# Kernel tuning notes

Hardware: AMD Instinct MI355X
Metric: run time of the kernel (lower is better)

The kernel has to match this reference:

```python
import jax, jax.numpy as jnp
import numpy as np

B, N, K, H, NI = 8, 4096, 32, 128, 384
SCALE = 30.0
EPS = 1e-5


def _ln(x, g, b):
    m = jnp.mean(x, axis=-1, keepdims=True)
    v = jnp.mean(jnp.square(x - m), axis=-1, keepdims=True)
    return (x - m) * jax.lax.rsqrt(v + EPS) * g + b


def setup_inputs() -> dict:
    key = jax.random.key(0)
    ks = jax.random.split(key, 20)
    w = lambda k, shape: jax.random.normal(k, shape, jnp.float32) * 0.02
    return {
        "h_V": jax.random.normal(ks[0], (B, N, H), jnp.float32),
        "h_E": jax.random.normal(ks[1], (B, N, K, NI), jnp.float32),
        "mask_V": (jax.random.uniform(ks[2], (B, N)) > 0.1).astype(jnp.float32),
        "mask_attend": (jax.random.uniform(ks[3], (B, N, K)) > 0.1).astype(jnp.float32),
        "W1_w": w(ks[4], (H, H + NI)), "W1_b": jnp.zeros((H,), jnp.float32),
        "W2_w": w(ks[5], (H, H)), "W2_b": jnp.zeros((H,), jnp.float32),
        "W3_w": w(ks[6], (H, H)), "W3_b": jnp.zeros((H,), jnp.float32),
        "ln1_g": jnp.ones((H,), jnp.float32), "ln1_b": jnp.zeros((H,), jnp.float32),
        "ln2_g": jnp.ones((H,), jnp.float32), "ln2_b": jnp.zeros((H,), jnp.float32),
        "Win_w": w(ks[7], (4 * H, H)), "Win_b": jnp.zeros((4 * H,), jnp.float32),
        "Wout_w": w(ks[8], (H, 4 * H)), "Wout_b": jnp.zeros((H,), jnp.float32),
    }


def reference(h_V, h_E, mask_V, mask_attend,
              W1_w, W1_b, W2_w, W2_b, W3_w, W3_b,
              ln1_g, ln1_b, ln2_g, ln2_b,
              Win_w, Win_b, Wout_w, Wout_b):
    gelu = lambda x: jax.nn.gelu(x, approximate=False)  # torch exact GELU
    # Split W1 across the broadcast (h_V) and per-edge (h_E) inputs instead of
    # materializing the [B,N,K,H+NI] concat: identical math, less memory.
    W1v, W1e = W1_w[:, :H], W1_w[:, H:]
    hv_part = jnp.einsum('bnh,oh->bno', h_V, W1v)              # [B,N,H]
    he_part = jnp.einsum('bnke,oe->bnko', h_E, W1e)            # [B,N,K,H]
    m = gelu(hv_part[:, :, None, :] + he_part + W1_b)
    m = gelu(jnp.einsum('bnkh,oh->bnko', m, W2_w) + W2_b)
    m = jnp.einsum('bnkh,oh->bnko', m, W3_w) + W3_b            # h_message
    m = mask_attend[..., None] * m
    dh = jnp.sum(m, axis=-2) / SCALE                           # [B,N,H]
    h = _ln(h_V + dh, ln1_g, ln1_b)
    ff = jnp.einsum('bnf,of->bno', gelu(jnp.einsum('bnh,fh->bnf', h, Win_w) + Win_b), Wout_w) + Wout_b
    h = _ln(h + ff, ln2_g, ln2_b)
    return mask_V[..., None] * h
```

## Files before the change

### kernel.cpp

```cpp
#include <hip/hip_runtime.h>

#define NODES 32768

typedef __attribute__((ext_vector_type(8))) short bf16x8;
typedef __attribute__((ext_vector_type(4))) float f32x4;

__device__ __forceinline__ unsigned short f2bf(float f) {
  __bf16 b = (__bf16)f;
  return __builtin_bit_cast(unsigned short, b);
}

__device__ __forceinline__ float gelu_f(float x) {
  float e = __builtin_amdgcn_exp2f(-2.4558673f * x);
  return x * __builtin_amdgcn_rcpf(1.0f + e);
}

__device__ __forceinline__ f32x4 mfma16(bf16x8 a, bf16x8 b, f32x4 c) {
  return __builtin_amdgcn_mfma_f32_16x16x32_bf16(a, b, c, 0, 0, 0);
}

__global__ void DecLayer_54357106098674_kernel() {}

__global__ __launch_bounds__(256) void pack_kernel(
    const float* __restrict__ W, unsigned short* __restrict__ out,
    int ctiles, int ld) {
  int ct = blockIdx.x % ctiles;
  int ks = blockIdx.x / ctiles;
#pragma unroll
  for (int h = 0; h < 2; ++h) {
    int idx = threadIdx.x + h * 256;
    int j = idx & 7;
    int lane = idx >> 3;
    int o = ct * 16 + (lane & 15);
    int k = ks * 32 + ((lane >> 4) << 3) + j;
    out[((size_t)blockIdx.x * 64 + lane) * 8 + j] = f2bf(W[(size_t)o * ld + k]);
  }
}

__global__ __launch_bounds__(256, 3) void edge_kernel(
    const float* __restrict__ hE, const float* __restrict__ hV,
    const float* __restrict__ maskA,
    const unsigned short* __restrict__ W1p,
    const unsigned short* __restrict__ W2p,
    const unsigned short* __restrict__ W3p,
    const float* __restrict__ W1bias,
    const float* __restrict__ W2bias, const float* __restrict__ W3bias,
    const float* __restrict__ ln1g, const float* __restrict__ ln1b,
    float* __restrict__ hb) {
  __shared__ __align__(16) unsigned short A[64 * 392];
  __shared__ __align__(16) unsigned short hvb[2][136];
  __shared__ float mkl[64];
  unsigned short* m1 = A;
  unsigned short* m2 = A + 8704;
  float* red2 = (float*)(A + 17408);

  const int t = threadIdx.x;
  const int pair = ((blockIdx.x & 7) << 11) | (blockIdx.x >> 3);
  const int node0 = pair * 2;
  const float* vb0 = hV + (size_t)node0 * 128;
  const float* vb1 = vb0 + 128;

  {
    const int rr = t >> 3, cc = t & 7;
    const f32x4* src = (const f32x4*)(hE + (size_t)node0 * 12288) + rr * 96 + cc;
    unsigned short* dst0 = &A[rr * 392 + cc * 4];
#pragma unroll
    for (int i = 0; i < 12; ++i) {
      f32x4 v = __builtin_nontemporal_load(src + i * 8);
      ushort4 u;
      u.x = f2bf(v[0]); u.y = f2bf(v[1]); u.z = f2bf(v[2]); u.w = f2bf(v[3]);
      *(ushort4*)(dst0 + i * 32) = u;
    }
    const f32x4* src1 = src + 32 * 96;
    unsigned short* dst1 = &A[(rr + 32) * 392 + cc * 4];
#pragma unroll
    for (int i = 0; i < 12; ++i) {
      f32x4 v = __builtin_nontemporal_load(src1 + i * 8);
      ushort4 u;
      u.x = f2bf(v[0]); u.y = f2bf(v[1]); u.z = f2bf(v[2]); u.w = f2bf(v[3]);
      *(ushort4*)(dst1 + i * 32) = u;
    }
  }
  if (t < 64) {
    int nn = t >> 5, s = t & 31;
    f32x4 v = ((const f32x4*)(hV + (size_t)(node0 + nn) * 128))[s];
    ushort4 u;
    u.x = f2bf(v[0]); u.y = f2bf(v[1]); u.z = f2bf(v[2]); u.w = f2bf(v[3]);
    *(ushort4*)&hvb[nn][s * 4] = u;
  } else if (t < 128) {
    int q = t - 64;
    mkl[q] = maskA[(size_t)node0 * 32 + q];
  }
  __syncthreads();

  const int w = t >> 6, l = t & 63, lr = l & 15, lk = l >> 4;
  const int ct0 = w * 2, ct1 = w * 2 + 1;
  const int c0 = ct0 * 16 + lr, c1 = ct1 * 16 + lr;

  f32x4 g0[4], g1[4];
#pragma unroll
  for (int rt = 0; rt < 4; ++rt) {
    g0[rt] = (f32x4){0.f, 0.f, 0.f, 0.f};
    g1[rt] = (f32x4){0.f, 0.f, 0.f, 0.f};
  }
#pragma unroll
  for (int ks = 0; ks < 16; ++ks) {
    bf16x8 w0 = *(const bf16x8*)&W1p[((size_t)(ks * 8 + ct0) * 64 + l) * 8];
    bf16x8 w1 = *(const bf16x8*)&W1p[((size_t)(ks * 8 + ct1) * 64 + l) * 8];
#pragma unroll
    for (int rt = 0; rt < 4; ++rt) {
      bf16x8 a;
      if (ks < 4)
        a = *(const bf16x8*)&hvb[rt >> 1][ks * 32 + lk * 8];
      else
        a = *(const bf16x8*)&A[(rt * 16 + lr) * 392 + (ks - 4) * 32 + lk * 8];
      g0[rt] = mfma16(a, w0, g0[rt]);
      g1[rt] = mfma16(a, w1, g1[rt]);
    }
  }
  __syncthreads();

  {
    float bb0 = W1bias[c0], bb1 = W1bias[c1];
#pragma unroll
    for (int rt = 0; rt < 4; ++rt) {
#pragma unroll
      for (int r = 0; r < 4; ++r) {
        int row = rt * 16 + lk * 4 + r;
        m1[row * 136 + c0] = f2bf(gelu_f(g0[rt][r] + bb0));
        m1[row * 136 + c1] = f2bf(gelu_f(g1[rt][r] + bb1));
      }
    }
  }
  __syncthreads();

  f32x4 d0[4], d1[4];
#pragma unroll
  for (int rt = 0; rt < 4; ++rt) {
    d0[rt] = (f32x4){0.f, 0.f, 0.f, 0.f};
    d1[rt] = (f32x4){0.f, 0.f, 0.f, 0.f};
  }
#pragma unroll
  for (int ks = 0; ks < 4; ++ks) {
    bf16x8 w0 = *(const bf16x8*)&W2p[((size_t)(ks * 8 + ct0) * 64 + l) * 8];
    bf16x8 w1 = *(const bf16x8*)&W2p[((size_t)(ks * 8 + ct1) * 64 + l) * 8];
#pragma unroll
    for (int rt = 0; rt < 4; ++rt) {
      bf16x8 a = *(const bf16x8*)&m1[(rt * 16 + lr) * 136 + ks * 32 + lk * 8];
      d0[rt] = mfma16(a, w0, d0[rt]);
      d1[rt] = mfma16(a, w1, d1[rt]);
    }
  }
  {
    float bb0 = W2bias[c0], bb1 = W2bias[c1];
#pragma unroll
    for (int rt = 0; rt < 4; ++rt) {
#pragma unroll
      for (int r = 0; r < 4; ++r) {
        int row = rt * 16 + lk * 4 + r;
        m2[row * 136 + c0] = f2bf(gelu_f(d0[rt][r] + bb0));
        m2[row * 136 + c1] = f2bf(gelu_f(d1[rt][r] + bb1));
      }
    }
  }
  __syncthreads();

  f32x4 e0[4], e1[4];
#pragma unroll
  for (int rt = 0; rt < 4; ++rt) {
    e0[rt] = (f32x4){0.f, 0.f, 0.f, 0.f};
    e1[rt] = (f32x4){0.f, 0.f, 0.f, 0.f};
  }
#pragma unroll
  for (int ks = 0; ks < 4; ++ks) {
    bf16x8 w0 = *(const bf16x8*)&W3p[((size_t)(ks * 8 + ct0) * 64 + l) * 8];
    bf16x8 w1 = *(const bf16x8*)&W3p[((size_t)(ks * 8 + ct1) * 64 + l) * 8];
#pragma unroll
    for (int rt = 0; rt < 4; ++rt) {
      bf16x8 a = *(const bf16x8*)&m2[(rt * 16 + lr) * 136 + ks * 32 + lk * 8];
      e0[rt] = mfma16(a, w0, e0[rt]);
      e1[rt] = mfma16(a, w1, e1[rt]);
    }
  }

  {
    float b30 = W3bias[c0], b31 = W3bias[c1];
    float cs00 = 0.f, cs01 = 0.f, cs10 = 0.f, cs11 = 0.f;
#pragma unroll
    for (int r = 0; r < 4; ++r) {
      float mka = mkl[lk * 4 + r];
      float mkb = mkl[16 + lk * 4 + r];
      float mkc = mkl[32 + lk * 4 + r];
      float mkd = mkl[48 + lk * 4 + r];
      cs00 += mka * (e0[0][r] + b30) + mkb * (e0[1][r] + b30);
      cs01 += mka * (e1[0][r] + b31) + mkb * (e1[1][r] + b31);
      cs10 += mkc * (e0[2][r] + b30) + mkd * (e0[3][r] + b30);
      cs11 += mkc * (e1[2][r] + b31) + mkd * (e1[3][r] + b31);
    }
    cs00 += __shfl_xor(cs00, 16); cs00 += __shfl_xor(cs00, 32);
    cs01 += __shfl_xor(cs01, 16); cs01 += __shfl_xor(cs01, 32);
    cs10 += __shfl_xor(cs10, 16); cs10 += __shfl_xor(cs10, 32);
    cs11 += __shfl_xor(cs11, 16); cs11 += __shfl_xor(cs11, 32);
    if (lk == 0) {
      red2[c0]       = vb0[c0] + cs00 * (1.0f / 30.0f);
      red2[c1]       = vb0[c1] + cs01 * (1.0f / 30.0f);
      red2[128 + c0] = vb1[c0] + cs10 * (1.0f / 30.0f);
      red2[128 + c1] = vb1[c1] + cs11 * (1.0f / 30.0f);
    }
  }
  __syncthreads();

  {
    const int nn = w >> 1, ww = w & 1;
    const float* rn = red2 + nn * 128;
    float v0 = rn[l], v1 = rn[l + 64];
    float s = v0 + v1, sq = v0 * v0 + v1 * v1;
#pragma unroll
    for (int off = 1; off < 64; off <<= 1) {
      s += __shfl_xor(s, off);
      sq += __shfl_xor(sq, off);
    }
    float mean = s * (1.0f / 128.0f);
    float var = sq * (1.0f / 128.0f) - mean * mean;
    float rs = rsqrtf(var + 1e-5f);
    size_t ob = (size_t)(node0 + nn) * 128;
    if (ww == 0)
      hb[ob + l] = (v0 - mean) * rs * ln1g[l] + ln1b[l];
    else
      hb[ob + 64 + l] = (v1 - mean) * rs * ln1g[64 + l] + ln1b[64 + l];
  }
}

__global__ __launch_bounds__(256) void ffn_kernel(
    const float* h,
    const unsigned short* __restrict__ Winp,
    const unsigned short* __restrict__ Woutp,
    const float* __restrict__ Winbias, const float* __restrict__ Woutbias,
    const float* __restrict__ ln2g, const float* __restrict__ ln2b,
    const float* __restrict__ maskV, float* out) {
  __shared__ __align__(16) unsigned short hA[32 * 136];
  __shared__ __align__(16) unsigned short tl[32 * 520];
  __shared__ float mn[32], rstd[32], mv[32];
  float* ol = (float*)tl;

  const int t = threadIdx.x;
  const size_t base = (size_t)blockIdx.x * 32 * 128;

#pragma unroll
  for (int i = 0; i < 4; ++i) {
    int q = t + i * 256;
    int row = q >> 5, c4 = q & 31;
    f32x4 v = ((const f32x4*)(h + base))[q];
    ushort4 u;
    u.x = f2bf(v[0]); u.y = f2bf(v[1]); u.z = f2bf(v[2]); u.w = f2bf(v[3]);
    *(ushort4*)&hA[row * 136 + c4 * 4] = u;
  }
  if (t < 32) mv[t] = maskV[(size_t)blockIdx.x * 32 + t];
  __syncthreads();

  const int w = t >> 6, l = t & 63, lr = l & 15, lk = l >> 4;

  f32x4 p0[8], p1[8];
#pragma unroll
  for (int j = 0; j < 8; ++j) { p0[j] = (f32x4){0.f,0.f,0.f,0.f}; p1[j] = (f32x4){0.f,0.f,0.f,0.f}; }
#pragma unroll
  for (int ks = 0; ks < 4; ++ks) {
    bf16x8 a0 = *(const bf16x8*)&hA[lr * 136 + ks * 32 + lk * 8];
    bf16x8 a1 = *(const bf16x8*)&hA[(16 + lr) * 136 + ks * 32 + lk * 8];
#pragma unroll
    for (int j = 0; j < 8; ++j) {
      bf16x8 bv = *(const bf16x8*)&Winp[((size_t)(ks * 32 + (w * 8 + j)) * 64 + l) * 8];
      p0[j] = mfma16(a0, bv, p0[j]);
      p1[j] = mfma16(a1, bv, p1[j]);
    }
  }
#pragma unroll
  for (int j = 0; j < 8; ++j) {
    int col = (w * 8 + j) * 16 + lr;
    float bb = Winbias[col];
#pragma unroll
    for (int r = 0; r < 4; ++r) {
      tl[(lk * 4 + r) * 520 + col] = f2bf(gelu_f(p0[j][r] + bb));
      tl[(16 + lk * 4 + r) * 520 + col] = f2bf(gelu_f(p1[j][r] + bb));
    }
  }
  __syncthreads();

  const int ct0 = w * 2, ct1 = w * 2 + 1;
  const int c0 = ct0 * 16 + lr, c1 = ct1 * 16 + lr;
  f32x4 d00 = {0.f,0.f,0.f,0.f}, d01 = {0.f,0.f,0.f,0.f};
  f32x4 d10 = {0.f,0.f,0.f,0.f}, d11 = {0.f,0.f,0.f,0.f};
#pragma unroll
  for (int ks = 0; ks < 16; ++ks) {
    bf16x8 a0 = *(const bf16x8*)&tl[lr * 520 + ks * 32 + lk * 8];
    bf16x8 a1 = *(const bf16x8*)&tl[(16 + lr) * 520 + ks * 32 + lk * 8];
    bf16x8 w0 = *(const bf16x8*)&Woutp[((size_t)(ks * 8 + ct0) * 64 + l) * 8];
    bf16x8 w1 = *(const bf16x8*)&Woutp[((size_t)(ks * 8 + ct1) * 64 + l) * 8];
    d00 = mfma16(a0, w0, d00);
    d01 = mfma16(a0, w1, d01);
    d10 = mfma16(a1, w0, d10);
    d11 = mfma16(a1, w1, d11);
  }
  __syncthreads();
  {
    float bo0 = Woutbias[c0], bo1 = Woutbias[c1];
#pragma unroll
    for (int r = 0; r < 4; ++r) {
      int r0 = lk * 4 + r, r1 = 16 + lk * 4 + r;
      ol[r0 * 132 + c0] = d00[r] + bo0 + h[base + (size_t)r0 * 128 + c0];
      ol[r0 * 132 + c1] = d01[r] + bo1 + h[base + (size_t)r0 * 128 + c1];
      ol[r1 * 132 + c0] = d10[r] + bo0 + h[base + (size_t)r1 * 128 + c0];
      ol[r1 * 132 + c1] = d11[r] + bo1 + h[base + (size_t)r1 * 128 + c1];
    }
  }
  __syncthreads();

  {
    int row = t >> 3, p = t & 7;
    float s = 0.f, sq = 0.f;
#pragma unroll
    for (int i = 0; i < 16; ++i) {
      float x = ol[row * 132 + p * 16 + i];
      s += x; sq += x * x;
    }
    s += __shfl_xor(s, 1); sq += __shfl_xor(sq, 1);
    s += __shfl_xor(s, 2); sq += __shfl_xor(sq, 2);
    s += __shfl_xor(s, 4); sq += __shfl_xor(sq, 4);
    if (p == 0) {
      float mean = s * (1.0f / 128.0f);
      mn[row] = mean;
      rstd[row] = rsqrtf(sq * (1.0f / 128.0f) - mean * mean + 1e-5f);
    }
  }
  __syncthreads();

#pragma unroll
  for (int i = 0; i < 4; ++i) {
    int q = t + i * 256;
    int row = q >> 5, c = (q & 31) * 4;
    float m_ = mn[row], rs_ = rstd[row], mvv = mv[row];
    const float* orow = &ol[row * 132];
    f32x4 o;
    o[0] = mvv * ((orow[c + 0] - m_) * rs_ * ln2g[c + 0] + ln2b[c + 0]);
    o[1] = mvv * ((orow[c + 1] - m_) * rs_ * ln2g[c + 1] + ln2b[c + 1]);
    o[2] = mvv * ((orow[c + 2] - m_) * rs_ * ln2g[c + 2] + ln2b[c + 2]);
    o[3] = mvv * ((orow[c + 3] - m_) * rs_ * ln2g[c + 3] + ln2b[c + 3]);
    ((f32x4*)(out + base))[q] = o;
  }
}

extern "C" void kernel_launch(void* const* d_in, const int* in_sizes, int n_in,
                              void* d_out, int out_size, void* d_ws, size_t ws_size,
                              hipStream_t stream) {
  (void)in_sizes; (void)n_in; (void)out_size; (void)ws_size;
  const float* h_V   = (const float*)d_in[0];
  const float* h_E   = (const float*)d_in[1];
  const float* maskV = (const float*)d_in[2];
  const float* maskA = (const float*)d_in[3];
  const float* W1w   = (const float*)d_in[4];
  const float* W1b   = (const float*)d_in[5];
  const float* W2w   = (const float*)d_in[6];
  const float* W2b   = (const float*)d_in[7];
  const float* W3w   = (const float*)d_in[8];
  const float* W3b   = (const float*)d_in[9];
  const float* g1    = (const float*)d_in[10];
  const float* b1    = (const float*)d_in[11];
  const float* g2    = (const float*)d_in[12];
  const float* b2    = (const float*)d_in[13];
  const float* Winw  = (const float*)d_in[14];
  const float* Winb  = (const float*)d_in[15];
  const float* Woutw = (const float*)d_in[16];
  const float* Woutb = (const float*)d_in[17];
  float* out = (float*)d_out;

  char* ws = (char*)d_ws;
  unsigned short* W1p   = (unsigned short*)(ws + 0);
  unsigned short* W2p   = (unsigned short*)(ws + 131072);
  unsigned short* W3p   = (unsigned short*)(ws + 163840);
  unsigned short* Winp  = (unsigned short*)(ws + 196608);
  unsigned short* Woutp = (unsigned short*)(ws + 327680);

  pack_kernel<<<128, 256, 0, stream>>>(W1w,   W1p,    8, 512);
  pack_kernel<<<32,  256, 0, stream>>>(W2w,   W2p,    8, 128);
  pack_kernel<<<32,  256, 0, stream>>>(W3w,   W3p,    8, 128);
  pack_kernel<<<128, 256, 0, stream>>>(Winw,  Winp,  32, 128);
  pack_kernel<<<128, 256, 0, stream>>>(Woutw, Woutp,  8, 512);

  edge_kernel<<<NODES / 2, 256, 0, stream>>>(h_E, h_V, maskA, W1p, W2p, W3p,
                                             W1b, W2b, W3b, g1, b1, out);
  ffn_kernel<<<NODES / 32, 256, 0, stream>>>(out, Winp, Woutp, Winb, Woutb,
                                             g2, b2, maskV, out);
}
```

Before: 436.6 us.

## Switch edge MLP h_E, W1e, W2, W3 and activations to FP8 MFMA

```diff
diff --git a/kernel.cpp b/kernel.cpp
--- a/kernel.cpp
+++ b/kernel.cpp
@@ -10,6 +10,16 @@
   return __builtin_bit_cast(unsigned short, b);
 }
 
+__device__ __forceinline__ unsigned char f2fp8(float x) {
+  int v = __builtin_amdgcn_cvt_pk_fp8_f32(x, x, 0, false);
+  return (unsigned char)(v & 0xff);
+}
+__device__ __forceinline__ unsigned int pk4(f32x4 v) {
+  int r = __builtin_amdgcn_cvt_pk_fp8_f32(v[0], v[1], 0, false);
+  r = __builtin_amdgcn_cvt_pk_fp8_f32(v[2], v[3], r, true);
+  return (unsigned int)r;
+}
+
 __device__ __forceinline__ float gelu_f(float x) {
   float e = __builtin_amdgcn_exp2f(-2.4558673f * x);
   return x * __builtin_amdgcn_rcpf(1.0f + e);
@@ -18,12 +28,15 @@
 __device__ __forceinline__ f32x4 mfma16(bf16x8 a, bf16x8 b, f32x4 c) {
   return __builtin_amdgcn_mfma_f32_16x16x32_bf16(a, b, c, 0, 0, 0);
 }
+__device__ __forceinline__ f32x4 mfma8(long a, long b, f32x4 c) {
+  return __builtin_amdgcn_mfma_f32_16x16x32_fp8_fp8(a, b, c, 0, 0, 0);
+}
 
 __global__ void DecLayer_54357106098674_kernel() {}
 
 __global__ __launch_bounds__(256) void pack_kernel(
     const float* __restrict__ W, unsigned short* __restrict__ out,
-    int ctiles, int ld) {
+    int ctiles, int ld, int koff) {
   int ct = blockIdx.x % ctiles;
   int ks = blockIdx.x / ctiles;
 #pragma unroll
@@ -33,26 +46,43 @@
     int lane = idx >> 3;
     int o = ct * 16 + (lane & 15);
     int k = ks * 32 + ((lane >> 4) << 3) + j;
-    out[((size_t)blockIdx.x * 64 + lane) * 8 + j] = f2bf(W[(size_t)o * ld + k]);
-  }
-}
-
-__global__ __launch_bounds__(256, 3) void edge_kernel(
+    out[((size_t)blockIdx.x * 64 + lane) * 8 + j] = f2bf(W[(size_t)o * ld + koff + k]);
+  }
+}
+
+__global__ __launch_bounds__(256) void pack8_kernel(
+    const float* __restrict__ W, unsigned char* __restrict__ out,
+    int ctiles, int ld, int koff) {
+  int ct = blockIdx.x % ctiles;
+  int ks = blockIdx.x / ctiles;
+#pragma unroll
+  for (int h = 0; h < 2; ++h) {
+    int idx = threadIdx.x + h * 256;
+    int j = idx & 7;
+    int lane = idx >> 3;
+    int o = ct * 16 + (lane & 15);
+    int k = ks * 32 + ((lane >> 4) << 3) + j;
+    out[((size_t)blockIdx.x * 64 + lane) * 8 + j] = f2fp8(W[(size_t)o * ld + koff + k]);
+  }
+}
+
+__global__ __launch_bounds__(256, 6) void edge_kernel(
     const float* __restrict__ hE, const float* __restrict__ hV,
     const float* __restrict__ maskA,
-    const unsigned short* __restrict__ W1p,
-    const unsigned short* __restrict__ W2p,
-    const unsigned short* __restrict__ W3p,
+    const unsigned short* __restrict__ W1vp,
+    const unsigned char* __restrict__ W1e8,
+    const unsigned char* __restrict__ W2p8,
+    const unsigned char* __restrict__ W3p8,
     const float* __restrict__ W1bias,
     const float* __restrict__ W2bias, const float* __restrict__ W3bias,
     const float* __restrict__ ln1g, const float* __restrict__ ln1b,
     float* __restrict__ hb) {
-  __shared__ __align__(16) unsigned short A[64 * 392];
+  __shared__ __align__(16) unsigned char A8[64 * 392];
   __shared__ __align__(16) unsigned short hvb[2][136];
   __shared__ float mkl[64];
-  unsigned short* m1 = A;
-  unsigned short* m2 = A + 8704;
-  float* red2 = (float*)(A + 17408);
+  unsigned char* m1 = A8;
+  unsigned char* m2 = A8 + 8704;
+  float* red2 = (float*)(A8 + 17408);
 
   const int t = threadIdx.x;
   const int pair = ((blockIdx.x & 7) << 11) | (blockIdx.x >> 3);
@@ -63,22 +93,18 @@
   {
     const int rr = t >> 3, cc = t & 7;
     const f32x4* src = (const f32x4*)(hE + (size_t)node0 * 12288) + rr * 96 + cc;
-    unsigned short* dst0 = &A[rr * 392 + cc * 4];
+    unsigned char* dst0 = &A8[rr * 392 + cc * 4];
 #pragma unroll
     for (int i = 0; i < 12; ++i) {
       f32x4 v = __builtin_nontemporal_load(src + i * 8);
-      ushort4 u;
-      u.x = f2bf(v[0]); u.y = f2bf(v[1]); u.z = f2bf(v[2]); u.w = f2bf(v[3]);
-      *(ushort4*)(dst0 + i * 32) = u;
+      *(unsigned int*)(dst0 + i * 32) = pk4(v);
     }
     const f32x4* src1 = src + 32 * 96;
-    unsigned short* dst1 = &A[(rr + 32) * 392 + cc * 4];
+    unsigned char* dst1 = &A8[(rr + 32) * 392 + cc * 4];
 #pragma unroll
     for (int i = 0; i < 12; ++i) {
       f32x4 v = __builtin_nontemporal_load(src1 + i * 8);
-      ushort4 u;
-      u.x = f2bf(v[0]); u.y = f2bf(v[1]); u.z = f2bf(v[2]); u.w = f2bf(v[3]);
-      *(ushort4*)(dst1 + i * 32) = u;
+      *(unsigned int*)(dst1 + i * 32) = pk4(v);
     }
   }
   if (t < 64) {
@@ -104,20 +130,27 @@
     g1[rt] = (f32x4){0.f, 0.f, 0.f, 0.f};
   }
 #pragma unroll
-  for (int ks = 0; ks < 16; ++ks) {
-    bf16x8 w0 = *(const bf16x8*)&W1p[((size_t)(ks * 8 + ct0) * 64 + l) * 8];
-    bf16x8 w1 = *(const bf16x8*)&W1p[((size_t)(ks * 8 + ct1) * 64 + l) * 8];
-#pragma unroll
-    for (int rt = 0; rt < 4; ++rt) {
-      bf16x8 a;
-      if (ks < 4)
-        a = *(const bf16x8*)&hvb[rt >> 1][ks * 32 + lk * 8];
-      else
-        a = *(const bf16x8*)&A[(rt * 16 + lr) * 392 + (ks - 4) * 32 + lk * 8];
+  for (int ks = 0; ks < 4; ++ks) {
+    bf16x8 w0 = *(const bf16x8*)&W1vp[((size_t)(ks * 8 + ct0) * 64 + l) * 8];
+    bf16x8 w1 = *(const bf16x8*)&W1vp[((size_t)(ks * 8 + ct1) * 64 + l) * 8];
+#pragma unroll
+    for (int rt = 0; rt < 4; ++rt) {
+      bf16x8 a = *(const bf16x8*)&hvb[rt >> 1][ks * 32 + lk * 8];
       g0[rt] = mfma16(a, w0, g0[rt]);
       g1[rt] = mfma16(a, w1, g1[rt]);
     }
   }
+#pragma unroll
+  for (int ks = 0; ks < 12; ++ks) {
+    long w0 = *(const long*)&W1e8[((size_t)(ks * 8 + ct0) * 64 + l) * 8];
+    long w1 = *(const long*)&W1e8[((size_t)(ks * 8 + ct1) * 64 + l) * 8];
+#pragma unroll
+    for (int rt = 0; rt < 4; ++rt) {
+      long a = *(const long*)&A8[(rt * 16 + lr) * 392 + ks * 32 + lk * 8];
+      g0[rt] = mfma8(a, w0, g0[rt]);
+      g1[rt] = mfma8(a, w1, g1[rt]);
+    }
+  }
   __syncthreads();
 
   {
@@ -127,8 +160,8 @@
 #pragma unroll
       for (int r = 0; r < 4; ++r) {
         int row = rt * 16 + lk * 4 + r;
-        m1[row * 136 + c0] = f2bf(gelu_f(g0[rt][r] + bb0));
-        m1[row * 136 + c1] = f2bf(gelu_f(g1[rt][r] + bb1));
+        m1[row * 136 + c0] = f2fp8(gelu_f(g0[rt][r] + bb0));
+        m1[row * 136 + c1] = f2fp8(gelu_f(g1[rt][r] + bb1));
       }
     }
   }
@@ -142,13 +175,13 @@
   }
 #pragma unroll
   for (int ks = 0; ks < 4; ++ks) {
-    bf16x8 w0 = *(const bf16x8*)&W2p[((size_t)(ks * 8 + ct0) * 64 + l) * 8];
-    bf16x8 w1 = *(const bf16x8*)&W2p[((size_t)(ks * 8 + ct1) * 64 + l) * 8];
-#pragma unroll
-    for (int rt = 0; rt < 4; ++rt) {
-      bf16x8 a = *(const bf16x8*)&m1[(rt * 16 + lr) * 136 + ks * 32 + lk * 8];
-      d0[rt] = mfma16(a, w0, d0[rt]);
-      d1[rt] = mfma16(a, w1, d1[rt]);
+    long w0 = *(const long*)&W2p8[((size_t)(ks * 8 + ct0) * 64 + l) * 8];
+    long w1 = *(const long*)&W2p8[((size_t)(ks * 8 + ct1) * 64 + l) * 8];
+#pragma unroll
+    for (int rt = 0; rt < 4; ++rt) {
+      long a = *(const long*)&m1[(rt * 16 + lr) * 136 + ks * 32 + lk * 8];
+      d0[rt] = mfma8(a, w0, d0[rt]);
+      d1[rt] = mfma8(a, w1, d1[rt]);
     }
   }
   {
@@ -158,8 +191,8 @@
 #pragma unroll
       for (int r = 0; r < 4; ++r) {
         int row = rt * 16 + lk * 4 + r;
-        m2[row * 136 + c0] = f2bf(gelu_f(d0[rt][r] + bb0));
-        m2[row * 136 + c1] = f2bf(gelu_f(d1[rt][r] + bb1));
+        m2[row * 136 + c0] = f2fp8(gelu_f(d0[rt][r] + bb0));
+        m2[row * 136 + c1] = f2fp8(gelu_f(d1[rt][r] + bb1));
       }
     }
   }
@@ -173,13 +206,13 @@
   }
 #pragma unroll
   for (int ks = 0; ks < 4; ++ks) {
-    bf16x8 w0 = *(const bf16x8*)&W3p[((size_t)(ks * 8 + ct0) * 64 + l) * 8];
-    bf16x8 w1 = *(const bf16x8*)&W3p[((size_t)(ks * 8 + ct1) * 64 + l) * 8];
-#pragma unroll
-    for (int rt = 0; rt < 4; ++rt) {
-      bf16x8 a = *(const bf16x8*)&m2[(rt * 16 + lr) * 136 + ks * 32 + lk * 8];
-      e0[rt] = mfma16(a, w0, e0[rt]);
-      e1[rt] = mfma16(a, w1, e1[rt]);
+    long w0 = *(const long*)&W3p8[((size_t)(ks * 8 + ct0) * 64 + l) * 8];
+    long w1 = *(const long*)&W3p8[((size_t)(ks * 8 + ct1) * 64 + l) * 8];
+#pragma unroll
+    for (int rt = 0; rt < 4; ++rt) {
+      long a = *(const long*)&m2[(rt * 16 + lr) * 136 + ks * 32 + lk * 8];
+      e0[rt] = mfma8(a, w0, e0[rt]);
+      e1[rt] = mfma8(a, w1, e1[rt]);
     }
   }
 
@@ -374,20 +407,23 @@
   float* out = (float*)d_out;
 
   char* ws = (char*)d_ws;
-  unsigned short* W1p   = (unsigned short*)(ws + 0);
-  unsigned short* W2p   = (unsigned short*)(ws + 131072);
-  unsigned short* W3p   = (unsigned short*)(ws + 163840);
-  unsigned short* Winp  = (unsigned short*)(ws + 196608);
-  unsigned short* Woutp = (unsigned short*)(ws + 327680);
-
-  pack_kernel<<<128, 256, 0, stream>>>(W1w,   W1p,    8, 512);
-  pack_kernel<<<32,  256, 0, stream>>>(W2w,   W2p,    8, 128);
-  pack_kernel<<<32,  256, 0, stream>>>(W3w,   W3p,    8, 128);
-  pack_kernel<<<128, 256, 0, stream>>>(Winw,  Winp,  32, 128);
-  pack_kernel<<<128, 256, 0, stream>>>(Woutw, Woutp,  8, 512);
-
-  edge_kernel<<<NODES / 2, 256, 0, stream>>>(h_E, h_V, maskA, W1p, W2p, W3p,
-                                             W1b, W2b, W3b, g1, b1, out);
+  unsigned short* W1vp  = (unsigned short*)(ws + 0);
+  unsigned short* Winp  = (unsigned short*)(ws + 32768);
+  unsigned short* Woutp = (unsigned short*)(ws + 163840);
+  unsigned char*  W1e8  = (unsigned char*)(ws + 294912);
+  unsigned char*  W2p8  = (unsigned char*)(ws + 344064);
+  unsigned char*  W3p8  = (unsigned char*)(ws + 360448);
+
+  pack_kernel <<<32,  256, 0, stream>>>(W1w,   W1vp,  8, 512, 0);
+  pack8_kernel<<<96,  256, 0, stream>>>(W1w,   W1e8,  8, 512, 128);
+  pack8_kernel<<<32,  256, 0, stream>>>(W2w,   W2p8,  8, 128, 0);
+  pack8_kernel<<<32,  256, 0, stream>>>(W3w,   W3p8,  8, 128, 0);
+  pack_kernel <<<128, 256, 0, stream>>>(Winw,  Winp, 32, 128, 0);
+  pack_kernel <<<128, 256, 0, stream>>>(Woutw, Woutp, 8, 512, 0);
+
+  edge_kernel<<<NODES / 2, 256, 0, stream>>>(h_E, h_V, maskA, W1vp, W1e8,
+                                             W2p8, W3p8, W1b, W2b, W3b,
+                                             g1, b1, out);
   ffn_kernel<<<NODES / 32, 256, 0, stream>>>(out, Winp, Woutp, Winb, Woutb,
                                              g2, b2, maskV, out);
 }
```

New measurement: 373.8 us. 1.17x faster.
